# Optimization experiments

Measured on AMD Instinct MI355X. Metric: run time of the kernel, lower is better.

The kernel has to match this reference:

```python
import jax, jax.numpy as jnp
import numpy as np
from jax import lax

WIN = 11  # window_size


def _uniform_filter_valid(x, win):
    """Separable uniform (box) filter, VALID padding. x: [B,1,H,W].
    Equivalent to scipy uniform_filter followed by skimage's pad-cropping,
    since cropped positions only use fully-interior windows."""
    kh = jnp.full((1, 1, win, 1), 1.0 / win, dtype=x.dtype)
    kw = jnp.full((1, 1, 1, win), 1.0 / win, dtype=x.dtype)
    dn = ('NCHW', 'OIHW', 'NCHW')
    x = lax.conv_general_dilated(x, kh, (1, 1), 'VALID', dimension_numbers=dn)
    x = lax.conv_general_dilated(x, kw, (1, 1), 'VALID', dimension_numbers=dn)
    return x


def _ssim_loss(pred, target, win):
    # skimage structural_similarity with gaussian_weights=False, data_range=1.0
    data_range = 1.0
    C1 = (0.01 * data_range) ** 2
    C2 = (0.03 * data_range) ** 2
    NP = win * win
    cov_norm = NP / (NP - 1.0)  # sample covariance correction

    uf = lambda z: _uniform_filter_valid(z, win)
    ux = uf(pred)
    uy = uf(target)
    uxx = uf(pred * pred)
    uyy = uf(target * target)
    uxy = uf(pred * target)

    vx = cov_norm * (uxx - ux * ux)
    vy = cov_norm * (uyy - uy * uy)
    vxy = cov_norm * (uxy - ux * uy)

    A1 = 2.0 * ux * uy + C1
    A2 = 2.0 * vxy + C2
    B1 = ux * ux + uy * uy + C1
    B2 = vx + vy + C2
    S = (A1 * A2) / (B1 * B2)

    # mean SSIM per image, then mean over batch (identical to flat mean here)
    return 1.0 - jnp.mean(S)


def setup_inputs() -> dict:
    key = jax.random.key(0)
    k1, k2 = jax.random.split(key)
    B, C, H, W = 32, 1, 512, 512
    pred = jax.random.uniform(k1, (B, C, H, W), dtype=jnp.float32)
    target = jax.random.uniform(k2, (B, C, H, W), dtype=jnp.float32)
    return {"pred": pred, "target": target}


def reference(pred, target):
    return _ssim_loss(pred, target, WIN)
```

## Files before the change

### kernel.cpp

```cpp
#include <hip/hip_runtime.h>


#define WW 512
#define OH 502
#define LS 180
#define NBANDS 13
#define BANDROWS 40

__global__ __launch_bounds__(256, 5)
void ssim_main(const float* __restrict__ Pg, const float* __restrict__ Tg,
               float* __restrict__ partial) {
    __shared__ float vs[32 * LS];

    const int tid = threadIdx.x;
    const int b   = blockIdx.x;
    const int img   = b / 39;
    const int rem   = b - img * 39;
    const int strip = rem / NBANDS;
    const int vb    = rem - strip * NBANDS;

    const int outw = (strip == 2) ? 166 : 168;
    const int inw  = outw + 10;
    const int col0 = strip * 168;
    const int y0   = vb * BANDROWS;
    const int rowsband = min(BANDROWS, OH - y0);

    const float* P = Pg + img * (WW * WW) + col0;
    const float* T = Tg + img * (WW * WW) + col0;

    const int k  = tid & 7;
    const int cg = tid >> 3;
    const int x0 = cg * 8;
    const int nout = outw - x0;

    const float NP  = 121.0f;
    const float cn  = 121.0f / 120.0f;
    const float C1n = 1e-4f * 121.0f * 121.0f;
    const float C2n = 9e-4f * 121.0f * 121.0f;

    float acc = 0.0f;

    for (int yb = y0; yb < y0 + rowsband; yb += 8) {
        const int rows = min(8, y0 + rowsband - yb);

        if (tid < inw) {
            const float* p0 = P + tid;
            const float* t0 = T + tid;
            float sp = 0.f, st = 0.f, sq = 0.f, sx = 0.f;
            float kp[7], kt[7];
            #pragma unroll
            for (int rr = 0; rr < 10; ++rr) {
                float p = p0[(yb + rr) * WW];
                float t = t0[(yb + rr) * WW];
                sp += p; st += t;
                sq = fmaf(p, p, sq); sq = fmaf(t, t, sq);
                sx = fmaf(p, t, sx);
                if (rr < 7) { kp[rr] = p; kt[rr] = t; }
            }
            #pragma unroll
            for (int kk = 0; kk < 8; ++kk) {
                if (kk < rows) {
                    float p = p0[(yb + 10 + kk) * WW];
                    float t = t0[(yb + 10 + kk) * WW];
                    sp += p; st += t;
                    sq = fmaf(p, p, sq); sq = fmaf(t, t, sq);
                    sx = fmaf(p, t, sx);
                    vs[(0 * 8 + kk) * LS + tid] = sp;
                    vs[(1 * 8 + kk) * LS + tid] = st;
                    vs[(2 * 8 + kk) * LS + tid] = sq;
                    vs[(3 * 8 + kk) * LS + tid] = sx;
                    if (kk < 7) {
                        float pp = kp[kk], tt = kt[kk];
                        sp -= pp; st -= tt;
                        sq = fmaf(pp, -pp, sq); sq = fmaf(tt, -tt, sq);
                        sx = fmaf(pp, -tt, sx);
                    }
                }
            }
        }
        __syncthreads();

        if (k < rows && nout > 0) {
            float wsum[4][8];
            #pragma unroll
            for (int q = 0; q < 4; ++q) {
                const float* base = &vs[(q * 8 + k) * LS + x0];
                float w[18];
                #pragma unroll
                for (int j4 = 0; j4 < 4; ++j4) {
                    float4 v = *(const float4*)(base + j4 * 4);
                    w[j4 * 4 + 0] = v.x; w[j4 * 4 + 1] = v.y;
                    w[j4 * 4 + 2] = v.z; w[j4 * 4 + 3] = v.w;
                }
                float2 v2 = *(const float2*)(base + 16);
                w[16] = v2.x; w[17] = v2.y;
                float s = 0.f;
                #pragma unroll
                for (int j = 0; j < 11; ++j) s += w[j];
                wsum[q][0] = s;
                #pragma unroll
                for (int i = 1; i < 8; ++i) { s += w[10 + i] - w[i - 1]; wsum[q][i] = s; }
            }
            #pragma unroll
            for (int i = 0; i < 8; ++i) {
                if (i < nout) {
                    float s0 = wsum[0][i], s1 = wsum[1][i];
                    float sqq = wsum[2][i], sxy = wsum[3][i];
                    float m1 = s0 * s1;
                    float q1 = fmaf(s1, s1, s0 * s0);
                    float A1 = fmaf(2.f, m1, C1n);
                    float B1 = q1 + C1n;
                    float t4 = fmaf(NP, sxy, -m1);
                    float A2 = fmaf(2.f * cn, t4, C2n);
                    float tB = fmaf(NP, sqq, -q1);
                    float B2 = fmaf(cn, tB, C2n);
                    acc = fmaf(A1 * A2, __builtin_amdgcn_rcpf(B1 * B2), acc);
                }
            }
        }
        __syncthreads();
    }

    #pragma unroll
    for (int off = 32; off > 0; off >>= 1) acc += __shfl_down(acc, off);
    if ((tid & 63) == 0) vs[tid >> 6] = acc;
    __syncthreads();
    if (tid == 0) partial[b] = vs[0] + vs[1] + vs[2] + vs[3];
}

__global__ __launch_bounds__(256)
void ssim_final(const float* __restrict__ partial, float* __restrict__ out) {
    __shared__ float wred[4];
    const int tid = threadIdx.x;
    float v = 0.f;
    #pragma unroll
    for (int j = 0; j < 5; ++j) {
        int idx = tid + j * 256;
        if (idx < 1248) v += partial[idx];
    }
    #pragma unroll
    for (int off = 32; off > 0; off >>= 1) v += __shfl_down(v, off);
    if ((tid & 63) == 0) wred[tid >> 6] = v;
    __syncthreads();
    if (tid == 0) {
        out[0] = 1.0f - (wred[0] + wred[1] + wred[2] + wred[3]) / 8064128.0f;
    }
}

extern "C" void kernel_launch(void* const* d_in, const int* in_sizes, int n_in,
                              void* d_out, int out_size, void* d_ws, size_t ws_size,
                              hipStream_t stream) {
    const float* pred = (const float*)d_in[0];
    const float* targ = (const float*)d_in[1];
    float* out     = (float*)d_out;
    float* partial = (float*)d_ws;

    ssim_main<<<dim3(1248), dim3(256), 0, stream>>>(pred, targ, partial);
    ssim_final<<<dim3(1), dim3(256), 0, stream>>>(partial, out);
}
```

Measured before the change: 116.2 us.

## Replace LDS strip tiling with per-wave DPP scans and atomic reduction

Each wave now owns a 54-column by 32-row tile. It keeps running vertical window sums in registers and forms the horizontal 11-wide box sums with a DPP inclusive wave scan plus one shuffle. This removes shared-memory staging and block barriers. The separate finalize kernel is replaced by a memset and one atomicAdd per block. The cost is more halo reloading, since 64 lanes yield only 54 outputs and each band re-reads 10 rows, and the atomics make the summation order nondeterministic.

```diff
diff --git a/kernel.cpp b/kernel.cpp
--- a/kernel.cpp
+++ b/kernel.cpp
@@ -3,147 +3,127 @@
 
 #define WW 512
 #define OH 502
-#define LS 180
-#define NBANDS 13
-#define BANDROWS 40
+#define BANDROWS 32
+#define INV_N (1.0f / 8064128.0f)
+
+#define DPP_ADD(x, ctrl, rmask)                                            \
+    x += __int_as_float(__builtin_amdgcn_update_dpp(                       \
+        0, __float_as_int(x), (ctrl), (rmask), 0xf, true))
+
+__device__ __forceinline__ float wave_iscan(float x) {
+    DPP_ADD(x, 0x111, 0xf);
+    DPP_ADD(x, 0x112, 0xf);
+    DPP_ADD(x, 0x114, 0xf);
+    DPP_ADD(x, 0x118, 0xf);
+    DPP_ADD(x, 0x142, 0xa);
+    DPP_ADD(x, 0x143, 0xc);
+    return x;
+}
 
 __global__ __launch_bounds__(256, 5)
 void ssim_main(const float* __restrict__ Pg, const float* __restrict__ Tg,
-               float* __restrict__ partial) {
-    __shared__ float vs[32 * LS];
+               float* __restrict__ outp) {
+    const int tid  = threadIdx.x;
+    const int lane = tid & 63;
+    const int wv   = tid >> 6;
+    const int Wid  = blockIdx.x * 4 + wv;
+    const int img   = Wid / 160;
+    const int rem   = Wid - img * 160;
+    const int strip = rem >> 4;
+    const int band  = rem & 15;
 
-    const int tid = threadIdx.x;
-    const int b   = blockIdx.x;
-    const int img   = b / 39;
-    const int rem   = b - img * 39;
-    const int strip = rem / NBANDS;
-    const int vb    = rem - strip * NBANDS;
+    const int col0 = (strip == 9) ? 448 : strip * 54;
+    const int y0   = band * BANDROWS;
+    const int y1   = min(OH, y0 + BANDROWS);
 
-    const int outw = (strip == 2) ? 166 : 168;
-    const int inw  = outw + 10;
-    const int col0 = strip * 168;
-    const int y0   = vb * BANDROWS;
-    const int rowsband = min(BANDROWS, OH - y0);
+    const int col    = col0 + lane;
+    const bool active = (lane < 54) && (col >= strip * 54) && (col <= 501);
 
-    const float* P = Pg + img * (WW * WW) + col0;
-    const float* T = Tg + img * (WW * WW) + col0;
+    const int base = img * (WW * WW) + col;
 
-    const int k  = tid & 7;
-    const int cg = tid >> 3;
-    const int x0 = cg * 8;
-    const int nout = outw - x0;
+    float sp = 0.f, st = 0.f, sq = 0.f, sx = 0.f;
+    {
+        int idx = base + y0 * WW;
+        #pragma unroll
+        for (int r = 0; r < 10; ++r) {
+            float p = Pg[idx], t = Tg[idx];
+            sp += p; st += t;
+            sq = fmaf(p, p, sq); sq = fmaf(t, t, sq);
+            sx = fmaf(p, t, sx);
+            idx += WW;
+        }
+    }
 
-    const float NP  = 121.0f;
-    const float cn  = 121.0f / 120.0f;
-    const float C1n = 1e-4f * 121.0f * 121.0f;
-    const float C2n = 9e-4f * 121.0f * 121.0f;
+    int in = base + (y0 + 10) * WW;
+    int io = base + y0 * WW;
+    float pn = Pg[in], tn = Tg[in];
+    float po = Pg[io], to = Tg[io];
 
-    float acc = 0.0f;
+    const float NP  = 121.f;
+    const float cn  = 121.f / 120.f;
+    const float C1n = 1e-4f * 121.f * 121.f;
+    const float C2n = 9e-4f * 121.f * 121.f;
 
-    for (int yb = y0; yb < y0 + rowsband; yb += 8) {
-        const int rows = min(8, y0 + rowsband - yb);
+    float acc = 0.f;
 
-        if (tid < inw) {
-            const float* p0 = P + tid;
-            const float* t0 = T + tid;
-            float sp = 0.f, st = 0.f, sq = 0.f, sx = 0.f;
-            float kp[7], kt[7];
-            #pragma unroll
-            for (int rr = 0; rr < 10; ++rr) {
-                float p = p0[(yb + rr) * WW];
-                float t = t0[(yb + rr) * WW];
-                sp += p; st += t;
-                sq = fmaf(p, p, sq); sq = fmaf(t, t, sq);
-                sx = fmaf(p, t, sx);
-                if (rr < 7) { kp[rr] = p; kt[rr] = t; }
-            }
-            #pragma unroll
-            for (int kk = 0; kk < 8; ++kk) {
-                if (kk < rows) {
-                    float p = p0[(yb + 10 + kk) * WW];
-                    float t = t0[(yb + 10 + kk) * WW];
-                    sp += p; st += t;
-                    sq = fmaf(p, p, sq); sq = fmaf(t, t, sq);
-                    sx = fmaf(p, t, sx);
-                    vs[(0 * 8 + kk) * LS + tid] = sp;
-                    vs[(1 * 8 + kk) * LS + tid] = st;
-                    vs[(2 * 8 + kk) * LS + tid] = sq;
-                    vs[(3 * 8 + kk) * LS + tid] = sx;
-                    if (kk < 7) {
-                        float pp = kp[kk], tt = kt[kk];
-                        sp -= pp; st -= tt;
-                        sq = fmaf(pp, -pp, sq); sq = fmaf(tt, -tt, sq);
-                        sx = fmaf(pp, -tt, sx);
-                    }
-                }
-            }
+    for (int y = y0; y < y1 - 1; ++y) {
+        sp += pn; st += tn;
+        sq = fmaf(pn, pn, sq); sq = fmaf(tn, tn, sq);
+        sx = fmaf(pn, tn, sx);
+        in += WW; io += WW;
+        float pn2 = Pg[in], tn2 = Tg[in];
+        float po2 = Pg[io], to2 = Tg[io];
+        float S0 = wave_iscan(sp), S1 = wave_iscan(st);
+        float S2 = wave_iscan(sq), S3 = wave_iscan(sx);
+        float W0 = __shfl(S0, lane + 10) - S0 + sp;
+        float W1 = __shfl(S1, lane + 10) - S1 + st;
+        float W2 = __shfl(S2, lane + 10) - S2 + sq;
+        float W3 = __shfl(S3, lane + 10) - S3 + sx;
+        if (active) {
+            float m1 = W0 * W1;
+            float q1 = fmaf(W0, W0, W1 * W1);
+            float A1 = fmaf(2.f, m1, C1n);
+            float B1 = q1 + C1n;
+            float A2 = fmaf(2.f * cn, fmaf(NP, W3, -m1), C2n);
+            float B2 = fmaf(cn, fmaf(NP, W2, -q1), C2n);
+            acc = fmaf(A1 * A2, __builtin_amdgcn_rcpf(B1 * B2), acc);
         }
-        __syncthreads();
-
-        if (k < rows && nout > 0) {
-            float wsum[4][8];
-            #pragma unroll
-            for (int q = 0; q < 4; ++q) {
-                const float* base = &vs[(q * 8 + k) * LS + x0];
-                float w[18];
-                #pragma unroll
-                for (int j4 = 0; j4 < 4; ++j4) {
-                    float4 v = *(const float4*)(base + j4 * 4);
-                    w[j4 * 4 + 0] = v.x; w[j4 * 4 + 1] = v.y;
-                    w[j4 * 4 + 2] = v.z; w[j4 * 4 + 3] = v.w;
-                }
-                float2 v2 = *(const float2*)(base + 16);
-                w[16] = v2.x; w[17] = v2.y;
-                float s = 0.f;
-                #pragma unroll
-                for (int j = 0; j < 11; ++j) s += w[j];
-                wsum[q][0] = s;
-                #pragma unroll
-                for (int i = 1; i < 8; ++i) { s += w[10 + i] - w[i - 1]; wsum[q][i] = s; }
-            }
-            #pragma unroll
-            for (int i = 0; i < 8; ++i) {
-                if (i < nout) {
-                    float s0 = wsum[0][i], s1 = wsum[1][i];
-                    float sqq = wsum[2][i], sxy = wsum[3][i];
-                    float m1 = s0 * s1;
-                    float q1 = fmaf(s1, s1, s0 * s0);
-                    float A1 = fmaf(2.f, m1, C1n);
-                    float B1 = q1 + C1n;
-                    float t4 = fmaf(NP, sxy, -m1);
-                    float A2 = fmaf(2.f * cn, t4, C2n);
-                    float tB = fmaf(NP, sqq, -q1);
-                    float B2 = fmaf(cn, tB, C2n);
-                    acc = fmaf(A1 * A2, __builtin_amdgcn_rcpf(B1 * B2), acc);
-                }
-            }
+        sp -= po; st -= to;
+        sq = fmaf(po, -po, sq); sq = fmaf(to, -to, sq);
+        sx = fmaf(po, -to, sx);
+        pn = pn2; tn = tn2; po = po2; to = to2;
+    }
+    {
+        sp += pn; st += tn;
+        sq = fmaf(pn, pn, sq); sq = fmaf(tn, tn, sq);
+        sx = fmaf(pn, tn, sx);
+        float S0 = wave_iscan(sp), S1 = wave_iscan(st);
+        float S2 = wave_iscan(sq), S3 = wave_iscan(sx);
+        float W0 = __shfl(S0, lane + 10) - S0 + sp;
+        float W1 = __shfl(S1, lane + 10) - S1 + st;
+        float W2 = __shfl(S2, lane + 10) - S2 + sq;
+        float W3 = __shfl(S3, lane + 10) - S3 + sx;
+        if (active) {
+            float m1 = W0 * W1;
+            float q1 = fmaf(W0, W0, W1 * W1);
+            float A1 = fmaf(2.f, m1, C1n);
+            float B1 = q1 + C1n;
+            float A2 = fmaf(2.f * cn, fmaf(NP, W3, -m1), C2n);
+            float B2 = fmaf(cn, fmaf(NP, W2, -q1), C2n);
+            acc = fmaf(A1 * A2, __builtin_amdgcn_rcpf(B1 * B2), acc);
         }
-        __syncthreads();
     }
 
     #pragma unroll
     for (int off = 32; off > 0; off >>= 1) acc += __shfl_down(acc, off);
-    if ((tid & 63) == 0) vs[tid >> 6] = acc;
-    __syncthreads();
-    if (tid == 0) partial[b] = vs[0] + vs[1] + vs[2] + vs[3];
-}
-
-__global__ __launch_bounds__(256)
-void ssim_final(const float* __restrict__ partial, float* __restrict__ out) {
     __shared__ float wred[4];
-    const int tid = threadIdx.x;
-    float v = 0.f;
-    #pragma unroll
-    for (int j = 0; j < 5; ++j) {
-        int idx = tid + j * 256;
-        if (idx < 1248) v += partial[idx];
-    }
-    #pragma unroll
-    for (int off = 32; off > 0; off >>= 1) v += __shfl_down(v, off);
-    if ((tid & 63) == 0) wred[tid >> 6] = v;
+    if (lane == 0) wred[wv] = acc;
     __syncthreads();
     if (tid == 0) {
-        out[0] = 1.0f - (wred[0] + wred[1] + wred[2] + wred[3]) / 8064128.0f;
+        float s = wred[0] + wred[1] + wred[2] + wred[3];
+        float contrib = -s * INV_N;
+        if (blockIdx.x == 0) contrib += 1.0f;
+        atomicAdd(outp, contrib);
     }
 }
 
@@ -152,9 +132,8 @@
                               hipStream_t stream) {
     const float* pred = (const float*)d_in[0];
     const float* targ = (const float*)d_in[1];
-    float* out     = (float*)d_out;
-    float* partial = (float*)d_ws;
+    float* out = (float*)d_out;
 
-    ssim_main<<<dim3(1248), dim3(256), 0, stream>>>(pred, targ, partial);
-    ssim_final<<<dim3(1), dim3(256), 0, stream>>>(partial, out);
+    hipMemsetAsync(out, 0, sizeof(float), stream);
+    ssim_main<<<dim3(1280), dim3(256), 0, stream>>>(pred, targ, out);
 }
```

After: 128.9 us. +10.9%, slower.
